# Performance work log

Hardware: AMD Instinct MI355X
Metric: run time of the kernel (lower is better)

The kernel has to match this reference:

```python
import jax, jax.numpy as jnp
import numpy as np

INPUT_DIM = 1024
OUTPUT_DIM = 1024
DEGREE = 8


def pentanacci_basis(x, degree):
    # x: [B, I] (already sigmoided). Returns [B, I, degree+1].
    # P0 = 0, P1 = 1, P2 = x, P3 = x, P4 = x^2,
    # Pn = x*P(n-1) + P(n-2) + P(n-3) + P(n-4) + P(n-5) for n >= 5
    zeros = jnp.zeros_like(x)
    ones = jnp.ones_like(x)
    seeds = [zeros, ones, x, x, x * x]
    basis = seeds[: degree + 1]
    for n in range(5, degree + 1):
        basis.append(x * basis[n - 1] + basis[n - 2] + basis[n - 3]
                     + basis[n - 4] + basis[n - 5])
    return jnp.stack(basis, axis=-1)


def setup_inputs() -> dict:
    key = jax.random.key(0)
    kx, kw = jax.random.split(key)
    x = jax.random.normal(kx, (4096, INPUT_DIM), dtype=jnp.float32)
    std = 1.0 / (INPUT_DIM * (DEGREE + 1))
    coeffs = std * jax.random.normal(kw, (INPUT_DIM, OUTPUT_DIM, DEGREE + 1),
                                     dtype=jnp.float32)
    return {"x": x, "coeffs": coeffs}


def reference(x, coeffs):
    degree = coeffs.shape[-1] - 1
    xs = jax.nn.sigmoid(x)                      # [B, I]
    basis = pentanacci_basis(xs, degree)        # [B, I, D+1]
    y = jnp.einsum('bid,iod->bo', basis, coeffs)  # [B, O]
    return y
```

## Files before the change

### kernel.cpp

```cpp
#include <hip/hip_runtime.h>
#include <stdint.h>

#define M_DIM 4096
#define I_DIM 1024
#define O_DIM 1024
#define KB 6
#define K_DIM (I_DIM * KB)
#define SPLITS 4

typedef __attribute__((ext_vector_type(8))) short short8;
typedef __attribute__((ext_vector_type(4))) float f32x4;
typedef __attribute__((ext_vector_type(4))) unsigned int u32x4;
typedef __attribute__((ext_vector_type(4))) float hfloat4;
typedef __attribute__((ext_vector_type(8))) _Float16 h16x8;
typedef __attribute__((ext_vector_type(4))) _Float16 h16x4;

__device__ __forceinline__ unsigned short f2bf(float f) {
  union { float f; unsigned int u; } v; v.f = f;
  unsigned int u = v.u;
  unsigned int r = (u + 0x7FFFu + ((u >> 16) & 1u)) >> 16;
  return (unsigned short)r;
}

__global__ __launch_bounds__(256) void k_prep(const float* __restrict__ x,
                                              const float* __restrict__ C,
                                              unsigned short* __restrict__ A,
                                              unsigned short* __restrict__ Bt,
                                              float* __restrict__ partB) {
  const int bid = blockIdx.x;
  if (bid < 2048) {
    int t = bid * 256 + threadIdx.x;
    long e0 = (long)t * 8;
    const hfloat4* xp = (const hfloat4*)(x + e0);
    hfloat4 v0 = xp[0], v1 = xp[1];
    float xv[8];
    xv[0]=v0[0]; xv[1]=v0[1]; xv[2]=v0[2]; xv[3]=v0[3];
    xv[4]=v1[0]; xv[5]=v1[1]; xv[6]=v1[2]; xv[7]=v1[3];
    unsigned short outv[48];
#pragma unroll
    for (int e = 0; e < 8; ++e) {
      float s  = 1.0f / (1.0f + __expf(-xv[e]));
      float b2 = s, b3 = s, b4 = s * s;
      float b5 = fmaf(s, b4, b3 + b2 + 1.0f);
      float b6 = fmaf(s, b5, b4 + b3 + b2 + 1.0f);
      float b7 = fmaf(s, b6, b5 + b4 + b3 + b2);
      float b8 = fmaf(s, b7, b6 + b5 + b4 + b3);
      outv[e*6+0] = f2bf(s);
      outv[e*6+1] = f2bf(b4);
      outv[e*6+2] = f2bf(b5);
      outv[e*6+3] = f2bf(b6);
      outv[e*6+4] = f2bf(b7);
      outv[e*6+5] = f2bf(b8);
    }
    u32x4* dst = (u32x4*)(A + e0 * KB);
    const u32x4* srcv = (const u32x4*)outv;
#pragma unroll
    for (int q = 0; q < 6; ++q) dst[q] = srcv[q];
  } else {
    __shared__ unsigned short tile[32 * 192];
    __shared__ float bred[256];
    int b = bid - 2048;
    int i0 = (b & 31) * 32, o0 = (b >> 5) * 32;
    int t = threadIdx.x;
    int ol = t & 31, ig = t >> 5;
    float bsum = 0.f;
#pragma unroll
    for (int r = 0; r < 4; ++r) {
      int il = ig + r * 8;
      const float* p = C + (size_t)(i0 + il) * (O_DIM * 9) + (size_t)(o0 + ol) * 9;
      float c1 = p[1];
      float c2 = p[2], c3 = p[3], c4 = p[4], c5 = p[5], c6 = p[6], c7 = p[7], c8 = p[8];
      bsum += c1;
      unsigned short* q = &tile[ol * 192 + il * 6];
      q[0] = f2bf(c2 + c3);
      q[1] = f2bf(c4);
      q[2] = f2bf(c5);
      q[3] = f2bf(c6);
      q[4] = f2bf(c7);
      q[5] = f2bf(c8);
    }
    bred[t] = bsum;
    __syncthreads();
    if (t < 32) {
      float s = 0.f;
#pragma unroll
      for (int g = 0; g < 8; ++g) s += bred[g * 32 + t];
      partB[(size_t)(b & 31) * O_DIM + o0 + t] = s;
    }
    const u32x4* lsrc = (const u32x4*)tile;
#pragma unroll
    for (int r = 0; r < 3; ++r) {
      int c = t + r * 256;
      int row = c / 24, off = c % 24;
      u32x4* gdst = (u32x4*)(Bt + (size_t)(o0 + row) * K_DIM + (size_t)i0 * 6 + off * 8);
      *gdst = lsrc[c];
    }
  }
}

__global__ __launch_bounds__(256) void k_bias2(const float* __restrict__ partB,
                                               float* __restrict__ bias) {
  int o = blockIdx.x * 256 + threadIdx.x;
  float s = 0.f;
#pragma unroll
  for (int ib = 0; ib < 32; ++ib) s += partB[(size_t)ib * O_DIM + o];
  bias[o] = s;
}

#define SBAR __builtin_amdgcn_sched_barrier(0)

template<bool SPLIT>
__global__ __launch_bounds__(512, 2) void k_gemm8(const unsigned short* __restrict__ A,
                                                  const unsigned short* __restrict__ B,
                                                  const float* __restrict__ bias,
                                                  _Float16* __restrict__ part,
                                                  float* __restrict__ out) {
  constexpr int CK = SPLIT ? (K_DIM / SPLITS) : K_DIM;
  constexpr int NT = CK / 64;
  constexpr int PPX = SPLIT ? 8 : 2;
  __shared__ char lds[131072];
  const int tid = threadIdx.x;
  const int lane = tid & 63, wid = tid >> 6;
  const int wm = wid >> 2, wn = wid & 3;
  const int l15 = lane & 15, lk = lane >> 4, l7 = lane & 7;
  const int flat = blockIdx.x + (blockIdx.y << 2) + (blockIdx.z << 6);
  const int xcd = flat & 7, slot = flat >> 3;
  const int panel = xcd * PPX + (slot >> 2);
  const int xn = slot & 3;
  const int ym = panel & 15, zk = panel >> 4;
  const int m0 = ym * 256, n0 = xn * 256;
  const size_t kb = (size_t)zk * CK;
  const int srow = tid >> 3;
  const int cg8 = (((tid & 7) ^ ((tid >> 3) & 7)) * 8);
  const int cx0 = (lk ^ l7) * 16;
  const int cx1 = ((4 + lk) ^ l7) * 16;
  const int arow = wm * 128 + l15;
  const int brow = wn * 64 + l15;

  auto gload = [&](const unsigned short* s, int ldsoff) {
    __builtin_amdgcn_global_load_lds((const __attribute__((address_space(1))) void*)s,
        (__attribute__((address_space(3))) void*)(lds + ldsoff), 16, 0, 0);
  };
  auto stageA = [&](int buf, int h, int kt2) {
    const unsigned short* s = A + (size_t)(m0 + h * 128 + srow) * K_DIM + kb + (size_t)kt2 * 64 + cg8;
    int d = buf * 65536 + h * 16384 + tid * 16;
    gload(s, d);
    gload(s + (size_t)64 * K_DIM, d + 8192);
  };
  auto stageB = [&](int buf, int h, int kt2) {
    const unsigned short* s = B + (size_t)(n0 + h * 128 + srow) * K_DIM + kb + (size_t)kt2 * 64 + cg8;
    int d = buf * 65536 + 32768 + h * 16384 + tid * 16;
    gload(s, d);
    gload(s + (size_t)64 * K_DIM, d + 8192);
  };

  short8 a0[8], b0v[4], a1[8], b1v[4];
  f32x4 acc[8][4];
#pragma unroll
  for (int i = 0; i < 8; ++i)
#pragma unroll
    for (int n = 0; n < 4; ++n)
#pragma unroll
      for (int j = 0; j < 4; ++j) acc[i][n][j] = 0.f;

  auto readK = [&](int buf, int cx, short8 (&av)[8], short8 (&bv)[4]) {
#pragma unroll
    for (int mi = 0; mi < 8; ++mi)
      av[mi] = *(const short8*)(lds + buf * 65536 + (arow + mi * 16) * 128 + cx);
#pragma unroll
    for (int ni = 0; ni < 4; ++ni)
      bv[ni] = *(const short8*)(lds + buf * 65536 + 32768 + (brow + ni * 16) * 128 + cx);
  };
  auto quadK = [&](short8 (&av)[8], short8 (&bv)[4]) {
#pragma unroll
    for (int mi = 0; mi < 8; ++mi)
#pragma unroll
      for (int ni = 0; ni < 4; ++ni)
        acc[mi][ni] = __builtin_amdgcn_mfma_f32_16x16x32_bf16(av[mi], bv[ni], acc[mi][ni], 0, 0, 0);
  };

  stageA(0, 0, 0); stageA(0, 1, 0); stageB(0, 0, 0); stageB(0, 1, 0);
  asm volatile("s_waitcnt vmcnt(0)" ::: "memory"); SBAR;
  __builtin_amdgcn_s_barrier(); SBAR;
  readK(0, cx0, a0, b0v);

#pragma unroll 1
  for (int kt = 0; kt < NT; ++kt) {
    const int buf = kt & 1, nb = buf ^ 1;
    if (kt + 1 < NT) {
      stageA(nb, 0, kt + 1); stageA(nb, 1, kt + 1);
      stageB(nb, 0, kt + 1); stageB(nb, 1, kt + 1);
    }
    readK(buf, cx1, a1, b1v);
    __builtin_amdgcn_s_setprio(1);
    quadK(a0, b0v);
    quadK(a1, b1v);
    __builtin_amdgcn_s_setprio(0); SBAR;
    asm volatile("s_waitcnt lgkmcnt(0)" ::: "memory"); SBAR;
    if (kt + 1 < NT) {
      asm volatile("s_waitcnt vmcnt(0)" ::: "memory"); SBAR;
      __builtin_amdgcn_s_barrier(); SBAR;
      readK(nb, cx0, a0, b0v);
    }
  }

  if (SPLIT) {
    _Float16* base = part + (size_t)zk * ((size_t)M_DIM * O_DIM);
    const int gb0 = (m0 >> 2) + wm * 32 + lk;
#pragma unroll
    for (int mi = 0; mi < 8; ++mi) {
      int g = gb0 + mi * 4;
#pragma unroll
      for (int ni = 0; ni < 4; ++ni) {
        int col = n0 + wn * 64 + ni * 16 + l15;
        h16x4 v;
#pragma unroll
        for (int j = 0; j < 4; ++j) v[j] = (_Float16)acc[mi][ni][j];
        *(h16x4*)(base + ((size_t)g * O_DIM + col) * 4) = v;
      }
    }
  } else {
#pragma unroll
    for (int mi = 0; mi < 8; ++mi) {
      int r0 = m0 + wm * 128 + mi * 16 + (lk << 2);
#pragma unroll
      for (int ni = 0; ni < 4; ++ni) {
        int col = n0 + wn * 64 + ni * 16 + l15;
        float bv = bias[col];
#pragma unroll
        for (int j = 0; j < 4; ++j)
          out[(size_t)(r0 + j) * O_DIM + col] = acc[mi][ni][j] + bv;
      }
    }
  }
}

__global__ __launch_bounds__(256) void k_reduce(const _Float16* __restrict__ part,
                                                const float* __restrict__ bias,
                                                float* __restrict__ out) {
  __shared__ float lt[4][512];
  const int b = blockIdx.x, tt = threadIdx.x;
  const size_t P = (size_t)M_DIM * O_DIM;
  size_t idx = (size_t)b * 2048 + (size_t)tt * 8;
  h16x8 s0 = *(const h16x8*)(part + idx);
  h16x8 s1 = *(const h16x8*)(part + P + idx);
  h16x8 s2 = *(const h16x8*)(part + 2 * P + idx);
  h16x8 s3 = *(const h16x8*)(part + 3 * P + idx);
  const int g = b >> 1;
  const int cbase = (b & 1) << 9;
  const int c0 = tt * 2;
  float bv0 = bias[cbase + c0], bv1 = bias[cbase + c0 + 1];
#pragma unroll
  for (int k = 0; k < 8; ++k) {
    float r = (((float)s0[k] + (float)s1[k]) + ((float)s2[k] + (float)s3[k]))
              + ((k < 4) ? bv0 : bv1);
    lt[k & 3][c0 + (k >> 2)] = r;
  }
  __syncthreads();
  const int rj = tt >> 6, lc = (tt & 63) * 8;
  f32x4 v0 = *(const f32x4*)&lt[rj][lc];
  f32x4 v1 = *(const f32x4*)&lt[rj][lc + 4];
  float* o = out + (size_t)(4 * g + rj) * O_DIM + cbase + lc;
  *(f32x4*)o = v0;
  *(f32x4*)(o + 4) = v1;
}

extern "C" void kernel_launch(void* const* d_in, const int* in_sizes, int n_in,
                              void* d_out, int out_size, void* d_ws, size_t ws_size,
                              hipStream_t stream) {
  const float* x      = (const float*)d_in[0];
  const float* coeffs = (const float*)d_in[1];
  float* out = (float*)d_out;
  char* ws = (char*)d_ws;
  const size_t offA     = 0;
  const size_t offB     = 50331648;
  const size_t offBias  = offB + 12582912;
  const size_t offPartB = offBias + 4096;
  const size_t offPart  = offPartB + 131072;
  const size_t needSplit = offPart + (size_t)SPLITS * M_DIM * O_DIM * 2;

  unsigned short* A  = (unsigned short*)(ws + offA);
  unsigned short* Bt = (unsigned short*)(ws + offB);
  float* bias        = (float*)(ws + offBias);
  float* partB       = (float*)(ws + offPartB);
  _Float16* part     = (_Float16*)(ws + offPart);

  k_prep<<<3072, 256, 0, stream>>>(x, coeffs, A, Bt, partB);
  k_bias2<<<4, 256, 0, stream>>>(partB, bias);

  if (ws_size >= needSplit) {
    k_gemm8<true><<<dim3(4, 16, SPLITS), 512, 0, stream>>>(A, Bt, bias, part, out);
    k_reduce<<<(M_DIM * O_DIM) / (256 * 8), 256, 0, stream>>>(part, bias, out);
  } else {
    k_gemm8<false><<<dim3(4, 16, 1), 512, 0, stream>>>(A, Bt, bias, part, out);
  }
}
```

Measured before the change: 86.21 us.

## Switch GEMM main loop to four-stage LDS ring with 32-wide K tiles

Halves the K tile from 64 to 32 and replaces the two-buffer scheme with a four-slot LDS ring. Up to three tiles are prefetched through global_load_lds, and waits use vmcnt(8) instead of draining all loads before each barrier. Each iteration now handles two tiles, and LDS reads are interleaved with MFMA blocks. The LDS swizzle is redone for the 64-byte row pitch. The aim is to hide global-load latency behind MFMAs, at the cost of twice as many barriers per unit of K. The fixed vmcnt(8) counts may not wait long enough in the tail iterations, where fewer loads are in flight.

```diff
diff --git a/kernel.cpp b/kernel.cpp
--- a/kernel.cpp
+++ b/kernel.cpp
@@ -116,13 +116,13 @@
                                                   _Float16* __restrict__ part,
                                                   float* __restrict__ out) {
   constexpr int CK = SPLIT ? (K_DIM / SPLITS) : K_DIM;
-  constexpr int NT = CK / 64;
+  constexpr int NT = CK / 32;
   constexpr int PPX = SPLIT ? 8 : 2;
   __shared__ char lds[131072];
   const int tid = threadIdx.x;
   const int lane = tid & 63, wid = tid >> 6;
   const int wm = wid >> 2, wn = wid & 3;
-  const int l15 = lane & 15, lk = lane >> 4, l7 = lane & 7;
+  const int l15 = lane & 15, lk = lane >> 4;
   const int flat = blockIdx.x + (blockIdx.y << 2) + (blockIdx.z << 6);
   const int xcd = flat & 7, slot = flat >> 3;
   const int panel = xcd * PPX + (slot >> 2);
@@ -130,10 +130,9 @@
   const int ym = panel & 15, zk = panel >> 4;
   const int m0 = ym * 256, n0 = xn * 256;
   const size_t kb = (size_t)zk * CK;
-  const int srow = tid >> 3;
-  const int cg8 = (((tid & 7) ^ ((tid >> 3) & 7)) * 8);
-  const int cx0 = (lk ^ l7) * 16;
-  const int cx1 = ((4 + lk) ^ l7) * 16;
+  const int srow = tid >> 2;
+  const int cg8 = (((tid & 3) ^ ((tid >> 3) & 3)) * 8);
+  const int cx = (lk ^ ((l15 >> 1) & 3)) * 16;
   const int arow = wm * 128 + l15;
   const int brow = wn * 64 + l15;
 
@@ -141,20 +140,17 @@
     __builtin_amdgcn_global_load_lds((const __attribute__((address_space(1))) void*)s,
         (__attribute__((address_space(3))) void*)(lds + ldsoff), 16, 0, 0);
   };
-  auto stageA = [&](int buf, int h, int kt2) {
-    const unsigned short* s = A + (size_t)(m0 + h * 128 + srow) * K_DIM + kb + (size_t)kt2 * 64 + cg8;
-    int d = buf * 65536 + h * 16384 + tid * 16;
-    gload(s, d);
-    gload(s + (size_t)64 * K_DIM, d + 8192);
-  };
-  auto stageB = [&](int buf, int h, int kt2) {
-    const unsigned short* s = B + (size_t)(n0 + h * 128 + srow) * K_DIM + kb + (size_t)kt2 * 64 + cg8;
-    int d = buf * 65536 + 32768 + h * 16384 + tid * 16;
-    gload(s, d);
-    gload(s + (size_t)64 * K_DIM, d + 8192);
-  };
-
-  short8 a0[8], b0v[4], a1[8], b1v[4];
+  auto stageAB = [&](int buf, int kt2) {
+    const unsigned short* sa = A + (size_t)(m0 + srow) * K_DIM + kb + (size_t)kt2 * 32 + cg8;
+    const unsigned short* sb = B + (size_t)(n0 + srow) * K_DIM + kb + (size_t)kt2 * 32 + cg8;
+    int d = buf * 32768 + tid * 16;
+    gload(sa, d);
+    gload(sa + (size_t)128 * K_DIM, d + 8192);
+    gload(sb, d + 16384);
+    gload(sb + (size_t)128 * K_DIM, d + 24576);
+  };
+
+  short8 aA[8], bA[4], aB[8], bB[4];
   f32x4 acc[8][4];
 #pragma unroll
   for (int i = 0; i < 8; ++i)
@@ -163,13 +159,13 @@
 #pragma unroll
       for (int j = 0; j < 4; ++j) acc[i][n][j] = 0.f;
 
-  auto readK = [&](int buf, int cx, short8 (&av)[8], short8 (&bv)[4]) {
+  auto readK = [&](int buf, short8 (&av)[8], short8 (&bv)[4]) {
 #pragma unroll
     for (int mi = 0; mi < 8; ++mi)
-      av[mi] = *(const short8*)(lds + buf * 65536 + (arow + mi * 16) * 128 + cx);
+      av[mi] = *(const short8*)(lds + buf * 32768 + (arow + mi * 16) * 64 + cx);
 #pragma unroll
     for (int ni = 0; ni < 4; ++ni)
-      bv[ni] = *(const short8*)(lds + buf * 65536 + 32768 + (brow + ni * 16) * 128 + cx);
+      bv[ni] = *(const short8*)(lds + buf * 32768 + 16384 + (brow + ni * 16) * 64 + cx);
   };
   auto quadK = [&](short8 (&av)[8], short8 (&bv)[4]) {
 #pragma unroll
@@ -179,29 +175,29 @@
         acc[mi][ni] = __builtin_amdgcn_mfma_f32_16x16x32_bf16(av[mi], bv[ni], acc[mi][ni], 0, 0, 0);
   };
 
-  stageA(0, 0, 0); stageA(0, 1, 0); stageB(0, 0, 0); stageB(0, 1, 0);
-  asm volatile("s_waitcnt vmcnt(0)" ::: "memory"); SBAR;
+  stageAB(0, 0); stageAB(1, 1); stageAB(2, 2);
+  asm volatile("s_waitcnt vmcnt(8)" ::: "memory"); SBAR;
   __builtin_amdgcn_s_barrier(); SBAR;
-  readK(0, cx0, a0, b0v);
+  readK(0, aA, bA);
 
 #pragma unroll 1
-  for (int kt = 0; kt < NT; ++kt) {
-    const int buf = kt & 1, nb = buf ^ 1;
-    if (kt + 1 < NT) {
-      stageA(nb, 0, kt + 1); stageA(nb, 1, kt + 1);
-      stageB(nb, 0, kt + 1); stageB(nb, 1, kt + 1);
-    }
-    readK(buf, cx1, a1, b1v);
+  for (int kt = 0; kt < NT; kt += 2) {
+    if (kt + 3 < NT) stageAB((kt + 3) & 3, kt + 3);
+    asm volatile("s_waitcnt lgkmcnt(0)" ::: "memory"); SBAR;
+    asm volatile("s_waitcnt vmcnt(8)" ::: "memory"); SBAR;
+    __builtin_amdgcn_s_barrier(); SBAR;
+    readK((kt + 1) & 3, aB, bB);
     __builtin_amdgcn_s_setprio(1);
-    quadK(a0, b0v);
-    quadK(a1, b1v);
+    quadK(aA, bA);
     __builtin_amdgcn_s_setprio(0); SBAR;
+    if (kt + 4 < NT) stageAB((kt + 4) & 3, kt + 4);
     asm volatile("s_waitcnt lgkmcnt(0)" ::: "memory"); SBAR;
-    if (kt + 1 < NT) {
-      asm volatile("s_waitcnt vmcnt(0)" ::: "memory"); SBAR;
-      __builtin_amdgcn_s_barrier(); SBAR;
-      readK(nb, cx0, a0, b0v);
-    }
+    asm volatile("s_waitcnt vmcnt(8)" ::: "memory"); SBAR;
+    __builtin_amdgcn_s_barrier(); SBAR;
+    if (kt + 2 < NT) readK((kt + 2) & 3, aA, bA);
+    __builtin_amdgcn_s_setprio(1);
+    quadK(aB, bB);
+    __builtin_amdgcn_s_setprio(0); SBAR;
   }
 
   if (SPLIT) {
```

Result: slower. 89.45 us (+3.8%).

## Load B operand directly from global into registers, halve LDS staging

Applied to the files above, without the earlier changes.

B tiles are no longer staged through LDS. Each wave loads its B fragments straight from global memory into registers every k-step, and only A is double-buffered in LDS, so shared memory drops from 128KB to 64KB. The goal is to cut LDS traffic and footprint. The trade-off is that B loads are no longer shared between the two M-waves that use the same columns, so global and L2 traffic for B goes up. Those loads are also only hidden inside the same iteration rather than prefetched one tile ahead, and the old pipelined A register prefetch is removed.

```diff
diff --git a/kernel.cpp b/kernel.cpp
--- a/kernel.cpp
+++ b/kernel.cpp
@@ -118,7 +118,7 @@
   constexpr int CK = SPLIT ? (K_DIM / SPLITS) : K_DIM;
   constexpr int NT = CK / 64;
   constexpr int PPX = SPLIT ? 8 : 2;
-  __shared__ char lds[131072];
+  __shared__ char lds[65536];
   const int tid = threadIdx.x;
   const int lane = tid & 63, wid = tid >> 6;
   const int wm = wid >> 2, wn = wid & 3;
@@ -135,7 +135,7 @@
   const int cx0 = (lk ^ l7) * 16;
   const int cx1 = ((4 + lk) ^ l7) * 16;
   const int arow = wm * 128 + l15;
-  const int brow = wn * 64 + l15;
+  const unsigned short* Bbase = B + (size_t)(n0 + wn * 64 + l15) * K_DIM + kb + lk * 8;
 
   auto gload = [&](const unsigned short* s, int ldsoff) {
     __builtin_amdgcn_global_load_lds((const __attribute__((address_space(1))) void*)s,
@@ -143,18 +143,12 @@
   };
   auto stageA = [&](int buf, int h, int kt2) {
     const unsigned short* s = A + (size_t)(m0 + h * 128 + srow) * K_DIM + kb + (size_t)kt2 * 64 + cg8;
-    int d = buf * 65536 + h * 16384 + tid * 16;
+    int d = buf * 32768 + h * 16384 + tid * 16;
     gload(s, d);
     gload(s + (size_t)64 * K_DIM, d + 8192);
   };
-  auto stageB = [&](int buf, int h, int kt2) {
-    const unsigned short* s = B + (size_t)(n0 + h * 128 + srow) * K_DIM + kb + (size_t)kt2 * 64 + cg8;
-    int d = buf * 65536 + 32768 + h * 16384 + tid * 16;
-    gload(s, d);
-    gload(s + (size_t)64 * K_DIM, d + 8192);
-  };
-
-  short8 a0[8], b0v[4], a1[8], b1v[4];
+
+  short8 av[8][2], bv[4][2];
   f32x4 acc[8][4];
 #pragma unroll
   for (int i = 0; i < 8; ++i)
@@ -163,44 +157,50 @@
 #pragma unroll
       for (int j = 0; j < 4; ++j) acc[i][n][j] = 0.f;
 
-  auto readK = [&](int buf, int cx, short8 (&av)[8], short8 (&bv)[4]) {
+  auto loadB = [&](int kt2) {
+    const unsigned short* sb = Bbase + (size_t)kt2 * 64;
+#pragma unroll
+    for (int ni = 0; ni < 4; ++ni)
+#pragma unroll
+      for (int kc = 0; kc < 2; ++kc)
+        bv[ni][kc] = *(const short8*)(sb + (size_t)(ni * 16) * K_DIM + kc * 32);
+  };
+  auto readA = [&](int buf) {
+#pragma unroll
+    for (int mi = 0; mi < 8; ++mi) {
+      int rb = buf * 32768 + (arow + mi * 16) * 128;
+      av[mi][0] = *(const short8*)(lds + rb + cx0);
+      av[mi][1] = *(const short8*)(lds + rb + cx1);
+    }
+  };
+  auto quad = [&]() {
 #pragma unroll
     for (int mi = 0; mi < 8; ++mi)
-      av[mi] = *(const short8*)(lds + buf * 65536 + (arow + mi * 16) * 128 + cx);
-#pragma unroll
-    for (int ni = 0; ni < 4; ++ni)
-      bv[ni] = *(const short8*)(lds + buf * 65536 + 32768 + (brow + ni * 16) * 128 + cx);
-  };
-  auto quadK = [&](short8 (&av)[8], short8 (&bv)[4]) {
-#pragma unroll
-    for (int mi = 0; mi < 8; ++mi)
 #pragma unroll
       for (int ni = 0; ni < 4; ++ni)
-        acc[mi][ni] = __builtin_amdgcn_mfma_f32_16x16x32_bf16(av[mi], bv[ni], acc[mi][ni], 0, 0, 0);
-  };
-
-  stageA(0, 0, 0); stageA(0, 1, 0); stageB(0, 0, 0); stageB(0, 1, 0);
+#pragma unroll
+        for (int kc = 0; kc < 2; ++kc)
+          acc[mi][ni] = __builtin_amdgcn_mfma_f32_16x16x32_bf16(av[mi][kc], bv[ni][kc],
+                                                                acc[mi][ni], 0, 0, 0);
+  };
+
+  stageA(0, 0, 0); stageA(0, 1, 0);
   asm volatile("s_waitcnt vmcnt(0)" ::: "memory"); SBAR;
   __builtin_amdgcn_s_barrier(); SBAR;
-  readK(0, cx0, a0, b0v);
 
 #pragma unroll 1
   for (int kt = 0; kt < NT; ++kt) {
     const int buf = kt & 1, nb = buf ^ 1;
-    if (kt + 1 < NT) {
-      stageA(nb, 0, kt + 1); stageA(nb, 1, kt + 1);
-      stageB(nb, 0, kt + 1); stageB(nb, 1, kt + 1);
-    }
-    readK(buf, cx1, a1, b1v);
+    loadB(kt);
+    if (kt + 1 < NT) { stageA(nb, 0, kt + 1); stageA(nb, 1, kt + 1); }
+    readA(buf);
     __builtin_amdgcn_s_setprio(1);
-    quadK(a0, b0v);
-    quadK(a1, b1v);
+    quad();
     __builtin_amdgcn_s_setprio(0); SBAR;
     asm volatile("s_waitcnt lgkmcnt(0)" ::: "memory"); SBAR;
     if (kt + 1 < NT) {
       asm volatile("s_waitcnt vmcnt(0)" ::: "memory"); SBAR;
       __builtin_amdgcn_s_barrier(); SBAR;
-      readK(nb, cx0, a0, b0v);
     }
   }
 
@@ -226,10 +226,10 @@
 #pragma unroll
       for (int ni = 0; ni < 4; ++ni) {
         int col = n0 + wn * 64 + ni * 16 + l15;
-        float bv = bias[col];
+        float bvv = bias[col];
 #pragma unroll
         for (int j = 0; j < 4; ++j)
-          out[(size_t)(r0 + j) * O_DIM + col] = acc[mi][ni][j] + bv;
+          out[(size_t)(r0 + j) * O_DIM + col] = acc[mi][ni][j] + bvv;
       }
     }
   }
```

Measured after the change: 119.0 us. +38.0%, slower.
